# Kernel optimization log

Measured on AMD Instinct MI355X. Metric: run time of the kernel, lower is better.

## Reference

```python
import jax, jax.numpy as jnp
import numpy as np

B, S, D, H, DQK, DH = 2, 2048, 1024, 16, 64, 64

def setup_inputs() -> dict:
    key = jax.random.key(0)
    ks = jax.random.split(key, 9)
    return {
        "x":  jax.random.normal(ks[0], (B, S, D), jnp.float32),
        "Wq": jax.random.normal(ks[1], (H, D, DQK), jnp.float32) * (D ** -0.5),
        "bq": jax.random.normal(ks[2], (H, DQK), jnp.float32) * 0.02,
        "Wk": jax.random.normal(ks[3], (H, D, DQK), jnp.float32) * (D ** -0.5),
        "bk": jax.random.normal(ks[4], (H, DQK), jnp.float32) * 0.02,
        "Wv": jax.random.normal(ks[5], (H, D, DH), jnp.float32) * (D ** -0.5),
        "bv": jax.random.normal(ks[6], (H, DH), jnp.float32) * 0.02,
        "Wo": jax.random.normal(ks[7], (D, D), jnp.float32) * (D ** -0.5),
        "bo": jax.random.normal(ks[8], (D,), jnp.float32) * 0.02,
    }

def reference(x, Wq, bq, Wk, bk, Wv, bv, Wo, bo):
    b, s, d = x.shape
    # per-head projections, all heads batched: [B,H,S,*]
    Q = jnp.einsum('bsd,hde->bhse', x, Wq) + bq[None, :, None, :]
    K = jnp.einsum('bsd,hde->bhse', x, Wk) + bk[None, :, None, :]
    V = jnp.einsum('bsd,hde->bhse', x, Wv) + bv[None, :, None, :]
    scores = jnp.einsum('bhse,bhte->bhst', Q, K) * (Q.shape[-1] ** -0.5)
    causal = jnp.tril(jnp.ones((s, s), bool))
    scores = jnp.where(causal, scores, -jnp.inf)  # mask add as in torch code
    attn = jax.nn.softmax(scores, axis=-1)        # dropout p=0 (eval)
    out = jnp.einsum('bhst,bhtd->bhsd', attn, V)
    # concat heads along feature dim (head order matches torch.cat)
    out = out.transpose(0, 2, 1, 3).reshape(b, s, -1)
    return out @ Wo + bo
```

## Files before the change

kernel.cpp:

```cpp
#include <hip/hip_runtime.h>
#include <stdint.h>

typedef __attribute__((ext_vector_type(8))) short bh8;
typedef __attribute__((ext_vector_type(4))) float f32x4;
typedef __attribute__((ext_vector_type(4))) unsigned short u16x4;
typedef __attribute__((ext_vector_type(8))) unsigned short u16x8;
typedef __attribute__((ext_vector_type(2))) unsigned int u32x2;

#define DEVI static __device__ __forceinline__

constexpr int B_ = 2, S_ = 2048, D_ = 1024, H_ = 16, E_ = 64;

constexpr size_t OFF_XB  = 0;
constexpr size_t OFF_WQT = OFF_XB  + (size_t)B_*S_*D_;
constexpr size_t OFF_WKT = OFF_WQT + (size_t)H_*E_*D_;
constexpr size_t OFF_WVT = OFF_WKT + (size_t)H_*E_*D_;
constexpr size_t OFF_WOT = OFF_WVT + (size_t)H_*E_*D_;
constexpr size_t OFF_Q   = OFF_WOT + (size_t)D_*D_;
constexpr size_t OFF_K   = OFF_Q   + (size_t)B_*H_*S_*E_;
constexpr size_t OFF_VT  = OFF_K   + (size_t)B_*H_*S_*E_;
constexpr size_t OFF_O   = OFF_VT  + (size_t)B_*H_*S_*E_;

DEVI unsigned short f2bf(float f) {
    union { float f; unsigned u; } v; v.f = f;
    unsigned u = v.u;
    return (unsigned short)((u + 0x7fffu + ((u >> 16) & 1u)) >> 16);
}

DEVI unsigned cvt_pk_bf16(float lo, float hi) {
    unsigned r;
    asm("v_cvt_pk_bf16_f32 %0, %1, %2" : "=v"(r) : "v"(lo), "v"(hi));
    return r;
}

DEVI void gload16(const void* g, void* l) {
    __builtin_amdgcn_global_load_lds(
        (const __attribute__((address_space(1))) unsigned int*)g,
        (__attribute__((address_space(3))) unsigned int*)l, 16, 0, 0);
}

DEVI f32x4 mfma16(bh8 a, bh8 b, f32x4 c) {
    return __builtin_amdgcn_mfma_f32_16x16x32_bf16(a, b, c, 0, 0, 0);
}

template<int N> DEVI void vm_barrier() {
    asm volatile("s_waitcnt vmcnt(%0)" :: "i"(N) : "memory");
    __builtin_amdgcn_s_barrier();
    __builtin_amdgcn_sched_barrier(0);
}
DEVI void post_barrier() {
    __builtin_amdgcn_sched_barrier(0);
    __builtin_amdgcn_s_barrier();
    __builtin_amdgcn_sched_barrier(0);
}

__global__ __launch_bounds__(256) void k_convert_x(const float* __restrict__ x,
                                                   unsigned short* __restrict__ ws) {
    const int i = blockIdx.x * 256 + threadIdx.x;
    const float4 v = ((const float4*)x)[i];
    u16x4 o = { f2bf(v.x), f2bf(v.y), f2bf(v.z), f2bf(v.w) };
    *(u16x4*)(ws + OFF_XB + (size_t)i * 4) = o;
}

__global__ __launch_bounds__(256) void k_transpose_w(const float* __restrict__ Wq,
                                                     const float* __restrict__ Wk,
                                                     const float* __restrict__ Wv,
                                                     const float* __restrict__ Wo,
                                                     unsigned short* __restrict__ ws) {
    const int xi = blockIdx.x;
    const int z  = blockIdx.y;
    const int t  = threadIdx.x;
    __shared__ __align__(16) unsigned short tile[64][72];

    const float* src; unsigned short* dst;
    int inCols, inBase, outBase;
    if (z < 3) {
        src = (z == 0) ? Wq : (z == 1) ? Wk : Wv;
        dst = ws + ((z == 0) ? OFF_WQT : (z == 1) ? OFF_WKT : OFF_WVT);
        inCols = 64;
        inBase = xi * 64 * 64;
        const int h = xi >> 4, dt = xi & 15;
        outBase = h * 65536 + dt * 64;
    } else {
        src = Wo; dst = ws + OFF_WOT;
        inCols = 1024;
        const int et = xi >> 4, dt = xi & 15;
        inBase  = (dt * 64) * 1024 + et * 64;
        outBase = (et * 64) * 1024 + dt * 64;
    }
#pragma unroll
    for (int v = 0; v < 4; ++v) {
        const int flat = v * 256 + t;
        const int i = flat >> 4, j4 = (flat & 15) * 4;
        const float4 val = *(const float4*)(src + inBase + i * inCols + j4);
        tile[i][j4 + 0] = f2bf(val.x);
        tile[i][j4 + 1] = f2bf(val.y);
        tile[i][j4 + 2] = f2bf(val.z);
        tile[i][j4 + 3] = f2bf(val.w);
    }
    __syncthreads();
    const int j = t >> 2, iseg = (t & 3) * 16;
    u16x8 p0, p1;
#pragma unroll
    for (int u = 0; u < 8; ++u) p0[u] = tile[iseg + u][j];
#pragma unroll
    for (int u = 0; u < 8; ++u) p1[u] = tile[iseg + 8 + u][j];
    *(u16x8*)(dst + outBase + (size_t)j * 1024 + iseg)     = p0;
    *(u16x8*)(dst + outBase + (size_t)j * 1024 + iseg + 8) = p1;
}

DEVI void gemm_tile_128x128(const unsigned short* __restrict__ A,
                            const unsigned short* __restrict__ Bw,
                            unsigned short* lds,
                            f32x4 acc[2][8]) {
    const int lane = threadIdx.x & 63;
    const int w    = threadIdx.x >> 6;
    const int lr = lane & 15, lg = lane >> 4;
    const unsigned short* a0 = A  + (size_t)((w * 2 + 0) * 16 + lr) * D_ + lg * 8;
    const unsigned short* a1 = A  + (size_t)((w * 2 + 1) * 16 + lr) * D_ + lg * 8;
    const unsigned short* b0 = Bw + (size_t)((w * 2 + 0) * 16 + lr) * D_ + lg * 8;
    const unsigned short* b1 = Bw + (size_t)((w * 2 + 1) * 16 + lr) * D_ + lg * 8;
    const int oA0 = (w * 2 + 0) * 512, oA1 = (w * 2 + 1) * 512;
    const int oB0 = 4096 + oA0,        oB1 = 4096 + oA1;

    auto stage = [&](int ks, int bufi) {
        unsigned short* base = lds + bufi * 8192;
        gload16(a0 + ks * 32, base + oA0);
        gload16(a1 + ks * 32, base + oA1);
        gload16(b0 + ks * 32, base + oB0);
        gload16(b1 + ks * 32, base + oB1);
    };

    stage(0, 0); stage(1, 1); stage(2, 2);
    for (int ks = 0; ks < 32; ++ks) {
        if (ks < 30)       vm_barrier<8>();
        else if (ks == 30) vm_barrier<4>();
        else               vm_barrier<0>();
        const unsigned short* base = lds + (ks % 3) * 8192;
        bh8 af0 = *(const bh8*)(base + (w * 2 + 0) * 512 + lane * 8);
        bh8 af1 = *(const bh8*)(base + (w * 2 + 1) * 512 + lane * 8);
#pragma unroll
        for (int nt = 0; nt < 8; ++nt) {
            bh8 bf = *(const bh8*)(base + 4096 + nt * 512 + lane * 8);
            acc[0][nt] = mfma16(af0, bf, acc[0][nt]);
            acc[1][nt] = mfma16(af1, bf, acc[1][nt]);
        }
        post_barrier();
        if (ks + 3 < 32) stage(ks + 3, ks % 3);
    }
}

__global__ __launch_bounds__(256, 3) void k_qkv(unsigned short* __restrict__ ws,
                                                const float* __restrict__ bq,
                                                const float* __restrict__ bk,
                                                const float* __restrict__ bv) {
    const int stile = blockIdx.x;
    const int ntile = blockIdx.y;
    const int row0  = stile * 128;
    const unsigned short* A  = ws + OFF_XB  + (size_t)row0 * D_;
    const unsigned short* Bw = ws + OFF_WQT + (size_t)ntile * 128 * D_;

    __shared__ __align__(16) unsigned short lds[3 * 8192];
    f32x4 acc[2][8];
#pragma unroll
    for (int i = 0; i < 2; ++i)
#pragma unroll
        for (int j = 0; j < 8; ++j) acc[i][j] = (f32x4){0.f, 0.f, 0.f, 0.f};

    gemm_tile_128x128(A, Bw, lds, acc);

    const int lane = threadIdx.x & 63, w = threadIdx.x >> 6;
    const int lr = lane & 15, lg = lane >> 4;
    const int srow0 = row0 + w * 32;
    const int b     = srow0 >> 11;
    const int sl0   = srow0 & (S_ - 1);
#pragma unroll
    for (int mt = 0; mt < 2; ++mt) {
#pragma unroll
        for (int nt = 0; nt < 8; ++nt) {
            const int gcol = ntile * 128 + nt * 16;
            const int mat  = gcol >> 10;
            const int h    = (gcol >> 6) & 15;
            const int e    = (gcol & 63) + lr;
            const int bh   = b * H_ + h;
            const float bia = ((mat == 0) ? bq : (mat == 1) ? bk : bv)[h * 64 + e];
            if (mat == 0) {
                u16x4 pk;
#pragma unroll
                for (int r = 0; r < 4; ++r)
                    pk[r] = f2bf((acc[mt][nt][r] + bia) * 0.1803368801f);
                const int sl = sl0 + mt * 16 + lg * 4;
                *(u16x4*)(ws + OFF_Q + ((size_t)(bh * E_ + e)) * S_ + sl) = pk;
            } else if (mat == 2) {
                u16x4 pk;
#pragma unroll
                for (int r = 0; r < 4; ++r) pk[r] = f2bf(acc[mt][nt][r] + bia);
                const int sl = sl0 + mt * 16 + lg * 4;
                *(u16x4*)(ws + OFF_VT + ((size_t)(bh * E_ + e)) * S_ + sl) = pk;
            } else {
#pragma unroll
                for (int r = 0; r < 4; ++r) {
                    const int sl = sl0 + mt * 16 + lg * 4 + r;
                    ws[OFF_K + ((size_t)bh * S_ + sl) * E_ + e] = f2bf(acc[mt][nt][r] + bia);
                }
            }
        }
    }
}

__global__ __launch_bounds__(256, 4) void k_attn(unsigned short* __restrict__ ws) {
    const int flat = blockIdx.x;
    const int j    = flat & 31;
    const int qt   = 31 - (flat >> 5);
    const int bh   = (j & 7) * 4 + (j >> 3);
    const int lane = threadIdx.x & 63, w = threadIdx.x >> 6;
    const int lr = lane & 15, lg = lane >> 4;
    const unsigned short* Qp = ws + OFF_Q  + (size_t)bh * E_ * S_;
    const unsigned short* Kp = ws + OFF_K  + (size_t)bh * S_ * E_;
    const unsigned short* Vp = ws + OFF_VT + (size_t)bh * E_ * S_;
    __shared__ __align__(16) unsigned short ldsK[2][8 * 512];
    __shared__ __align__(16) unsigned short ldsV[2][8 * 512];
    __shared__ __align__(16) unsigned short ldsP[4 * 1024];

    const int qbase = qt * 64 + w * 16;
    bh8 qf[2];
#pragma unroll
    for (int kg = 0; kg < 2; ++kg) {
        bh8 t;
#pragma unroll
        for (int i = 0; i < 8; ++i)
            t[i] = (short)Qp[(size_t)(kg * 32 + lg * 8 + i) * S_ + qbase + lr];
        qf[kg] = t;
    }

    f32x4 o[4];
    float m = -3.0e38f, l = 0.f;
#pragma unroll
    for (int i = 0; i < 4; ++i) o[i] = (f32x4){0.f, 0.f, 0.f, 0.f};

    auto stage = [&](int kt, int bufi) {
        const int sk0 = kt * 64;
#pragma unroll
        for (int u = 0; u < 2; ++u) {
            const int blk = w * 2 + u;
            const int ct = blk >> 1, kg = blk & 1;
            gload16(Kp + (size_t)(sk0 + ct * 16 + lr) * E_ + kg * 32 + lg * 8,
                    &ldsK[bufi][blk * 512]);
            gload16(Vp + (size_t)(ct * 16 + lr) * S_ + sk0 + kg * 32 + lg * 8,
                    &ldsV[bufi][blk * 512]);
        }
    };

    unsigned short* Pw = ldsP + w * 1024;

    stage(0, 0);
    if (qt >= 1) stage(1, 1);

    for (int kt = 0; kt <= qt; ++kt) {
        if (kt < qt) vm_barrier<4>();
        else         vm_barrier<0>();
        const int cur = kt & 1;
        const unsigned short* Kc = ldsK[cur];
        const unsigned short* Vc = ldsV[cur];

        f32x4 sc[4];
#pragma unroll
        for (int ct = 0; ct < 4; ++ct) sc[ct] = (f32x4){0.f, 0.f, 0.f, 0.f};
#pragma unroll
        for (int ct = 0; ct < 4; ++ct)
#pragma unroll
            for (int kg = 0; kg < 2; ++kg) {
                bh8 kf = *(const bh8*)(Kc + (ct * 2 + kg) * 512 + lane * 8);
                sc[ct] = mfma16(kf, qf[kg], sc[ct]);
            }
        if (kt == qt) {
#pragma unroll
            for (int ct = 0; ct < 4; ++ct) {
                const int skl = ct * 16 + lg * 4;
#pragma unroll
                for (int r = 0; r < 4; ++r)
                    if (skl + r > w * 16 + lr) sc[ct][r] = -3.0e38f;
            }
        }
        float mx = fmaxf(fmaxf(sc[0][0], sc[0][1]), fmaxf(sc[0][2], sc[0][3]));
#pragma unroll
        for (int ct = 1; ct < 4; ++ct)
            mx = fmaxf(mx, fmaxf(fmaxf(sc[ct][0], sc[ct][1]),
                                 fmaxf(sc[ct][2], sc[ct][3])));
        mx = fmaxf(mx, __shfl_xor(mx, 16, 64));
        mx = fmaxf(mx, __shfl_xor(mx, 32, 64));
        const bool need = mx > m + 8.0f;
        if (__any(need)) {
            const float mn = need ? mx : m;
            const float sf = __builtin_amdgcn_exp2f(m - mn);
            m = mn;
            l *= sf;
#pragma unroll
            for (int r = 0; r < 4; ++r) {
                const float sfq = __shfl(sf, (lane & 48) + lg * 4 + r, 64);
#pragma unroll
                for (int et = 0; et < 4; ++et) o[et][r] *= sfq;
            }
        }
        float rs = 0.f;
#pragma unroll
        for (int ct = 0; ct < 4; ++ct)
#pragma unroll
            for (int r = 0; r < 4; ++r) {
                float p = __builtin_amdgcn_exp2f(sc[ct][r] - m);
                sc[ct][r] = p;
                rs += p;
            }
        rs += __shfl_xor(rs, 16, 64);
        rs += __shfl_xor(rs, 32, 64);
        l += rs;
#pragma unroll
        for (int ct = 0; ct < 4; ++ct) {
            u32x2 pk = { cvt_pk_bf16(sc[ct][0], sc[ct][1]),
                         cvt_pk_bf16(sc[ct][2], sc[ct][3]) };
            const int addr = (ct >> 1) * 512 +
                             ((((ct & 1) * 2) + (lg >> 1)) * 16 + lr) * 8 + (lg & 1) * 4;
            *(u32x2*)(Pw + addr) = pk;
        }
#pragma unroll
        for (int skg = 0; skg < 2; ++skg) {
            bh8 pf = *(const bh8*)(Pw + skg * 512 + lane * 8);
#pragma unroll
            for (int et = 0; et < 4; ++et) {
                bh8 vf = *(const bh8*)(Vc + (et * 2 + skg) * 512 + lane * 8);
                o[et] = mfma16(pf, vf, o[et]);
            }
        }
        post_barrier();
        if (kt + 2 <= qt) stage(kt + 2, cur);
    }
    const int b = bh >> 4, hh = bh & 15;
#pragma unroll
    for (int r = 0; r < 4; ++r) {
        const float lq = __shfl(l, (lane & 48) + lg * 4 + r, 64);
        const float inv = 1.0f / lq;
        const int s = qbase + lg * 4 + r;
#pragma unroll
        for (int et = 0; et < 4; ++et)
            ws[OFF_O + ((size_t)(b * S_ + s)) * D_ + hh * E_ + et * 16 + lr] =
                f2bf(o[et][r] * inv);
    }
}

__global__ __launch_bounds__(256, 3) void k_oproj(const unsigned short* __restrict__ ws,
                                                  const float* __restrict__ bo,
                                                  float* __restrict__ out) {
    const int stile = blockIdx.x;
    const int ntile = blockIdx.y;
    const unsigned short* A  = ws + OFF_O   + (size_t)stile * 128 * D_;
    const unsigned short* Bw = ws + OFF_WOT + (size_t)ntile * 128 * D_;
    __shared__ __align__(16) unsigned short lds[3 * 8192];
    f32x4 acc[2][8];
#pragma unroll
    for (int i = 0; i < 2; ++i)
#pragma unroll
        for (int j = 0; j < 8; ++j) acc[i][j] = (f32x4){0.f, 0.f, 0.f, 0.f};

    gemm_tile_128x128(A, Bw, lds, acc);

    const int lane = threadIdx.x & 63, w = threadIdx.x >> 6;
    const int lr = lane & 15, lg = lane >> 4;
    const int r0 = stile * 128 + w * 32;
#pragma unroll
    for (int mt = 0; mt < 2; ++mt)
#pragma unroll
        for (int nt = 0; nt < 8; ++nt) {
            const int e = ntile * 128 + nt * 16 + lr;
            const float bia = bo[e];
#pragma unroll
            for (int r = 0; r < 4; ++r)
                out[(size_t)(r0 + mt * 16 + lg * 4 + r) * D_ + e] = acc[mt][nt][r] + bia;
        }
}

extern "C" void kernel_launch(void* const* d_in, const int* in_sizes, int n_in,
                              void* d_out, int out_size, void* d_ws, size_t ws_size,
                              hipStream_t stream) {
    const float* x  = (const float*)d_in[0];
    const float* Wq = (const float*)d_in[1];
    const float* bq = (const float*)d_in[2];
    const float* Wk = (const float*)d_in[3];
    const float* bk = (const float*)d_in[4];
    const float* Wv = (const float*)d_in[5];
    const float* bv = (const float*)d_in[6];
    const float* Wo = (const float*)d_in[7];
    const float* bo = (const float*)d_in[8];
    float* out = (float*)d_out;
    unsigned short* ws = (unsigned short*)d_ws;

    k_convert_x<<<dim3((B_ * S_ * D_) / 4 / 256), 256, 0, stream>>>(x, ws);
    k_transpose_w<<<dim3(256, 4), 256, 0, stream>>>(Wq, Wk, Wv, Wo, ws);
    k_qkv<<<dim3(32, 24), 256, 0, stream>>>(ws, bq, bk, bv);
    k_attn<<<dim3(1024), 256, 0, stream>>>(ws);
    k_oproj<<<dim3(32, 8), 256, 0, stream>>>(ws, bo, out);
}
```

Before: 129.0 us.

## Enlarge QKV projection GEMM tile to 128x256 with 2x2 wave layout

The QKV projection kernel now computes a 128x256 output tile per block instead of 128x128. Waves are arranged 2x2, and each wave accumulates 4x8 MFMA sub-tiles, so every LDS B-fragment read is reused across four A fragments. The grid is halved to 384 blocks, with a larger triple-buffered LDS stage and occupancy lowered to 2 blocks per CU. The aim is to cut LDS and global traffic per FLOP, but it adds register pressure and can leave uneven work across CUs.

```diff
diff --git a/kernel.cpp b/kernel.cpp
--- a/kernel.cpp
+++ b/kernel.cpp
@@ -109,6 +109,110 @@
     *(u16x8*)(dst + outBase + (size_t)j * 1024 + iseg + 8) = p1;
 }
 
+DEVI void gemm_tile_128x256(const unsigned short* __restrict__ A,
+                            const unsigned short* __restrict__ Bw,
+                            unsigned short* lds,
+                            f32x4 acc[4][8]) {
+    const int lane = threadIdx.x & 63;
+    const int w    = threadIdx.x >> 6;
+    const int wm   = w & 1, wn = w >> 1;
+    const int lr = lane & 15, lg = lane >> 4;
+    const unsigned short* a0 = A  + (size_t)((w * 2 + 0) * 16 + lr) * D_ + lg * 8;
+    const unsigned short* a1 = A  + (size_t)((w * 2 + 1) * 16 + lr) * D_ + lg * 8;
+    const unsigned short* b0 = Bw + (size_t)((w * 4 + 0) * 16 + lr) * D_ + lg * 8;
+    const unsigned short* b1 = Bw + (size_t)((w * 4 + 1) * 16 + lr) * D_ + lg * 8;
+    const unsigned short* b2 = Bw + (size_t)((w * 4 + 2) * 16 + lr) * D_ + lg * 8;
+    const unsigned short* b3 = Bw + (size_t)((w * 4 + 3) * 16 + lr) * D_ + lg * 8;
+    const int oA0 = (w * 2 + 0) * 512, oA1 = (w * 2 + 1) * 512;
+    const int oB  = 4096 + w * 4 * 512;
+
+    auto stage = [&](int ks, int bufi) {
+        unsigned short* base = lds + bufi * 12288;
+        gload16(a0 + ks * 32, base + oA0);
+        gload16(a1 + ks * 32, base + oA1);
+        gload16(b0 + ks * 32, base + oB + 0 * 512);
+        gload16(b1 + ks * 32, base + oB + 1 * 512);
+        gload16(b2 + ks * 32, base + oB + 2 * 512);
+        gload16(b3 + ks * 32, base + oB + 3 * 512);
+    };
+
+    stage(0, 0); stage(1, 1); stage(2, 2);
+    for (int ks = 0; ks < 32; ++ks) {
+        if (ks < 30)       vm_barrier<12>();
+        else if (ks == 30) vm_barrier<6>();
+        else               vm_barrier<0>();
+        const unsigned short* base = lds + (ks % 3) * 12288;
+        bh8 af[4];
+#pragma unroll
+        for (int mt = 0; mt < 4; ++mt)
+            af[mt] = *(const bh8*)(base + (wm * 4 + mt) * 512 + lane * 8);
+#pragma unroll
+        for (int nt = 0; nt < 8; ++nt) {
+            bh8 bf = *(const bh8*)(base + 4096 + (wn * 8 + nt) * 512 + lane * 8);
+#pragma unroll
+            for (int mt = 0; mt < 4; ++mt)
+                acc[mt][nt] = mfma16(af[mt], bf, acc[mt][nt]);
+        }
+        post_barrier();
+        if (ks + 3 < 32) stage(ks + 3, ks % 3);
+    }
+}
+
+__global__ __launch_bounds__(256, 2) void k_qkv(unsigned short* __restrict__ ws,
+                                                const float* __restrict__ bq,
+                                                const float* __restrict__ bk,
+                                                const float* __restrict__ bv) {
+    const int stile = blockIdx.x;
+    const int ntile = blockIdx.y;
+    const int row0  = stile * 128;
+    const unsigned short* A  = ws + OFF_XB  + (size_t)row0 * D_;
+    const unsigned short* Bw = ws + OFF_WQT + (size_t)ntile * 256 * D_;
+
+    __shared__ __align__(16) unsigned short lds[3 * 12288];
+    f32x4 acc[4][8];
+#pragma unroll
+    for (int i = 0; i < 4; ++i)
+#pragma unroll
+        for (int j = 0; j < 8; ++j) acc[i][j] = (f32x4){0.f, 0.f, 0.f, 0.f};
+
+    gemm_tile_128x256(A, Bw, lds, acc);
+
+    const int lane = threadIdx.x & 63, w = threadIdx.x >> 6;
+    const int wm = w & 1, wn = w >> 1;
+    const int lr = lane & 15, lg = lane >> 4;
+    const int b  = row0 >> 11;
+#pragma unroll
+    for (int mt = 0; mt < 4; ++mt) {
+        const int sl0 = ((row0 + wm * 64 + mt * 16) & (S_ - 1)) + lg * 4;
+#pragma unroll
+        for (int nt = 0; nt < 8; ++nt) {
+            const int gcol = ntile * 256 + wn * 128 + nt * 16;
+            const int mat  = gcol >> 10;
+            const int h    = (gcol >> 6) & 15;
+            const int e    = (gcol & 63) + lr;
+            const int bh   = b * H_ + h;
+            const float bia = ((mat == 0) ? bq : (mat == 1) ? bk : bv)[h * 64 + e];
+            if (mat == 0) {
+                u16x4 pk;
+#pragma unroll
+                for (int r = 0; r < 4; ++r)
+                    pk[r] = f2bf((acc[mt][nt][r] + bia) * 0.1803368801f);
+                *(u16x4*)(ws + OFF_Q + ((size_t)(bh * E_ + e)) * S_ + sl0) = pk;
+            } else if (mat == 2) {
+                u16x4 pk;
+#pragma unroll
+                for (int r = 0; r < 4; ++r) pk[r] = f2bf(acc[mt][nt][r] + bia);
+                *(u16x4*)(ws + OFF_VT + ((size_t)(bh * E_ + e)) * S_ + sl0) = pk;
+            } else {
+#pragma unroll
+                for (int r = 0; r < 4; ++r)
+                    ws[OFF_K + ((size_t)bh * S_ + sl0 + r) * E_ + e] =
+                        f2bf(acc[mt][nt][r] + bia);
+            }
+        }
+    }
+}
+
 DEVI void gemm_tile_128x128(const unsigned short* __restrict__ A,
                             const unsigned short* __restrict__ Bw,
                             unsigned short* lds,
@@ -147,64 +251,6 @@
         }
         post_barrier();
         if (ks + 3 < 32) stage(ks + 3, ks % 3);
-    }
-}
-
-__global__ __launch_bounds__(256, 3) void k_qkv(unsigned short* __restrict__ ws,
-                                                const float* __restrict__ bq,
-                                                const float* __restrict__ bk,
-                                                const float* __restrict__ bv) {
-    const int stile = blockIdx.x;
-    const int ntile = blockIdx.y;
-    const int row0  = stile * 128;
-    const unsigned short* A  = ws + OFF_XB  + (size_t)row0 * D_;
-    const unsigned short* Bw = ws + OFF_WQT + (size_t)ntile * 128 * D_;
-
-    __shared__ __align__(16) unsigned short lds[3 * 8192];
-    f32x4 acc[2][8];
-#pragma unroll
-    for (int i = 0; i < 2; ++i)
-#pragma unroll
-        for (int j = 0; j < 8; ++j) acc[i][j] = (f32x4){0.f, 0.f, 0.f, 0.f};
-
-    gemm_tile_128x128(A, Bw, lds, acc);
-
-    const int lane = threadIdx.x & 63, w = threadIdx.x >> 6;
-    const int lr = lane & 15, lg = lane >> 4;
-    const int srow0 = row0 + w * 32;
-    const int b     = srow0 >> 11;
-    const int sl0   = srow0 & (S_ - 1);
-#pragma unroll
-    for (int mt = 0; mt < 2; ++mt) {
-#pragma unroll
-        for (int nt = 0; nt < 8; ++nt) {
-            const int gcol = ntile * 128 + nt * 16;
-            const int mat  = gcol >> 10;
-            const int h    = (gcol >> 6) & 15;
-            const int e    = (gcol & 63) + lr;
-            const int bh   = b * H_ + h;
-            const float bia = ((mat == 0) ? bq : (mat == 1) ? bk : bv)[h * 64 + e];
-            if (mat == 0) {
-                u16x4 pk;
-#pragma unroll
-                for (int r = 0; r < 4; ++r)
-                    pk[r] = f2bf((acc[mt][nt][r] + bia) * 0.1803368801f);
-                const int sl = sl0 + mt * 16 + lg * 4;
-                *(u16x4*)(ws + OFF_Q + ((size_t)(bh * E_ + e)) * S_ + sl) = pk;
-            } else if (mat == 2) {
-                u16x4 pk;
-#pragma unroll
-                for (int r = 0; r < 4; ++r) pk[r] = f2bf(acc[mt][nt][r] + bia);
-                const int sl = sl0 + mt * 16 + lg * 4;
-                *(u16x4*)(ws + OFF_VT + ((size_t)(bh * E_ + e)) * S_ + sl) = pk;
-            } else {
-#pragma unroll
-                for (int r = 0; r < 4; ++r) {
-                    const int sl = sl0 + mt * 16 + lg * 4 + r;
-                    ws[OFF_K + ((size_t)bh * S_ + sl) * E_ + e] = f2bf(acc[mt][nt][r] + bia);
-                }
-            }
-        }
     }
 }
 
@@ -395,7 +441,7 @@
 
     k_convert_x<<<dim3((B_ * S_ * D_) / 4 / 256), 256, 0, stream>>>(x, ws);
     k_transpose_w<<<dim3(256, 4), 256, 0, stream>>>(Wq, Wk, Wv, Wo, ws);
-    k_qkv<<<dim3(32, 24), 256, 0, stream>>>(ws, bq, bk, bv);
+    k_qkv<<<dim3(32, 12), 256, 0, stream>>>(ws, bq, bk, bv);
     k_attn<<<dim3(1024), 256, 0, stream>>>(ws);
     k_oproj<<<dim3(32, 8), 256, 0, stream>>>(ws, bo, out);
 }
```

New measurement: 133.0 us. 3.0% more time.
